# Kernel tuning notes

Hardware: AMD Instinct MI355X
Metric: run time of the kernel (lower is better)

## Reference

```python
import jax, jax.numpy as jnp
import numpy as np

NUM_IMGS = 8192
NUM_CAPS = 8192
R = 7        # views per image
D = 256      # embedding dim


def setup_inputs() -> dict:
    key = jax.random.key(0)
    k1, k2 = jax.random.split(key)
    imgs = jax.random.normal(k1, (NUM_IMGS, R, D), dtype=jnp.float32)
    caps = jax.random.normal(k2, (NUM_CAPS, D), dtype=jnp.float32)
    return {"imgs": imgs, "caps": caps}


def reference(imgs, caps):
    # scores[i, r, c] = <imgs[i, r], caps[c]>  then max over views r
    # matches torch.matmul(imgs, caps.t()).max(1)[0]
    scores = jnp.einsum("ird,cd->irc", imgs, caps)  # [num_imgs, r, num_caps]
    return scores.max(axis=1)                        # [num_imgs, num_caps]
```

## Files before the change

kernel.cpp:

```cpp
#include <hip/hip_runtime.h>
#include <hip/hip_bf16.h>
#include <cstdint>
#include <cstddef>

#define NI 8192
#define NC 8192
#define RV 7
#define DD 256

typedef __bf16 bf16x8 __attribute__((ext_vector_type(8)));
typedef float  f32x4  __attribute__((ext_vector_type(4)));

#define IMGS_WS_BYTES (32u * 56u * 16384u)
#define CAPS_WS_OFF   IMGS_WS_BYTES
#define CAPS_WS_BYTES (64u * 65536u)
#define WS_NEEDED     ((size_t)(IMGS_WS_BYTES + CAPS_WS_BYTES))

static __device__ __forceinline__ unsigned pkbf(float x, float y) {
  unsigned a = __float_as_uint(x) + 0x8000u;
  unsigned b = __float_as_uint(y) + 0x8000u;
  return __builtin_amdgcn_perm(b, a, 0x07060302u);
}

static __device__ __forceinline__ void gload16(const void* g, void* l) {
  __builtin_amdgcn_global_load_lds(
      (const __attribute__((address_space(1))) void*)g,
      (__attribute__((address_space(3))) void*)l, 16, 0, 0);
}

__global__ __launch_bounds__(256)
void conv_imgs(const float* __restrict__ imgs, uint4* __restrict__ ws) {
  unsigned T = blockIdx.x * 256u + threadIdx.x;
  unsigned img = T / 224u;
  unsigned rem = T - img * 224u;
  unsigned r  = rem >> 5;
  unsigned ju = rem & 31u;
  const float* s = imgs + ((size_t)img * RV + r) * DD + ju * 8u;
  float4 a = *(const float4*)s;
  float4 b = *(const float4*)(s + 4);
  uint4 v = { pkbf(a.x, a.y), pkbf(a.z, a.w), pkbf(b.x, b.y), pkbf(b.z, b.w) };
  unsigned ib = img >> 8, lrow = img & 255u;
  unsigned j = ju >> 2, u = ju & 3u;
  unsigned t = r * 8u + j;
  unsigned byteoff = (ib * 56u + t) * 16384u + u * 4096u + lrow * 16u;
  ws[byteoff >> 4] = v;
}

__global__ __launch_bounds__(256)
void conv_caps(const float* __restrict__ caps, uint4* __restrict__ ws) {
  unsigned T = blockIdx.x * 256u + threadIdx.x;
  unsigned gr = T >> 5;
  unsigned ju = T & 31u;
  const float* s = caps + (size_t)gr * DD + ju * 8u;
  float4 a = *(const float4*)s;
  float4 b = *(const float4*)(s + 4);
  uint4 v = { pkbf(a.x, a.y), pkbf(a.z, a.w), pkbf(b.x, b.y), pkbf(b.z, b.w) };
  unsigned cb = gr >> 7, row = gr & 127u;
  unsigned byteoff = cb * 65536u + ju * 2048u + row * 16u;
  ws[byteoff >> 4] = v;
}

__global__ __launch_bounds__(512, 2)
void mvm_mfma(const char* __restrict__ wi, const char* __restrict__ wc,
              float* __restrict__ out)
{
  __shared__ __align__(1024) char lds[65536 + 4 * 16384];
  char* const ldsB = lds;
  char* const ldsA = lds + 65536;

  const int tid  = threadIdx.x;
  const int lane = tid & 63;
  const int wid  = tid >> 6;
  const int wr   = wid >> 1;
  const int wq   = wid & 1;

  const int bid = (int)blockIdx.x;
  const int swz = (bid & 7) * 256 + (bid >> 3);
  const int ib  = swz >> 6;
  const int cb  = swz & 63;

  const char* bsrc  = wc + (size_t)cb * 65536u;
  const char* abase = wi + (size_t)ib * (56u * 16384u);

  #pragma unroll
  for (int l = 0; l < 8; ++l)
    gload16(bsrc + tid * 16 + l * 8192, ldsB + wid * 1024 + l * 8192);
  #pragma unroll
  for (int c = 0; c < 3; ++c) {
    gload16(abase + c * 16384 + tid * 16,        ldsA + c * 16384 + wid * 1024);
    gload16(abase + c * 16384 + tid * 16 + 8192, ldsA + c * 16384 + wid * 1024 + 8192);
  }
  const char* ap = abase + 3 * 16384 + tid * 16;

  asm volatile("s_waitcnt vmcnt(4)" ::: "memory");
  __builtin_amdgcn_s_barrier();
  asm volatile("" ::: "memory");

  const int lrow = lane & 15;
  const int lu   = lane >> 4;
  char* const aB       = ldsA + lu * 4096 + (wr * 64 + lrow) * 16;
  const char* const bB = ldsB + lu * 2048 + (wq * 64 + lrow) * 16;

  f32x4 omax[4][4];
  #pragma unroll
  for (int m = 0; m < 4; ++m)
    #pragma unroll
    for (int n = 0; n < 4; ++n)
      #pragma unroll
      for (int e = 0; e < 4; ++e)
        omax[m][n][e] = -3.4e38f;

  f32x4 acc[4][4];

  for (int i = 0; i < RV; ++i) {
    #pragma unroll
    for (int m = 0; m < 4; ++m)
      #pragma unroll
      for (int n = 0; n < 4; ++n)
        acc[m][n] = (f32x4){0.f, 0.f, 0.f, 0.f};

    #pragma unroll
    for (int j = 0; j < 8; ++j) {
      const int p = j & 3;
      const int q = (j + 3) & 3;

      if (j < 7 || i < 6) {
        gload16(ap,        ldsA + q * 16384 + wid * 1024);
        gload16(ap + 8192, ldsA + q * 16384 + wid * 1024 + 8192);
        ap += 16384;
      }

      bf16x8 a0 = *(const bf16x8*)(aB + p * 16384 + 0 * 256);
      bf16x8 a1 = *(const bf16x8*)(aB + p * 16384 + 1 * 256);
      bf16x8 a2 = *(const bf16x8*)(aB + p * 16384 + 2 * 256);
      bf16x8 a3 = *(const bf16x8*)(aB + p * 16384 + 3 * 256);
      bf16x8 b0 = *(const bf16x8*)(bB + j * 8192 + 0 * 256);
      bf16x8 b1 = *(const bf16x8*)(bB + j * 8192 + 1 * 256);
      bf16x8 b2 = *(const bf16x8*)(bB + j * 8192 + 2 * 256);
      bf16x8 b3 = *(const bf16x8*)(bB + j * 8192 + 3 * 256);

      __builtin_amdgcn_s_barrier();
      asm volatile("" ::: "memory");

      __builtin_amdgcn_s_setprio(1);
      acc[0][0] = __builtin_amdgcn_mfma_f32_16x16x32_bf16(a0, b0, acc[0][0], 0, 0, 0);
      acc[1][0] = __builtin_amdgcn_mfma_f32_16x16x32_bf16(a1, b0, acc[1][0], 0, 0, 0);
      acc[2][0] = __builtin_amdgcn_mfma_f32_16x16x32_bf16(a2, b0, acc[2][0], 0, 0, 0);
      acc[3][0] = __builtin_amdgcn_mfma_f32_16x16x32_bf16(a3, b0, acc[3][0], 0, 0, 0);
      acc[0][1] = __builtin_amdgcn_mfma_f32_16x16x32_bf16(a0, b1, acc[0][1], 0, 0, 0);
      acc[1][1] = __builtin_amdgcn_mfma_f32_16x16x32_bf16(a1, b1, acc[1][1], 0, 0, 0);
      acc[2][1] = __builtin_amdgcn_mfma_f32_16x16x32_bf16(a2, b1, acc[2][1], 0, 0, 0);
      acc[3][1] = __builtin_amdgcn_mfma_f32_16x16x32_bf16(a3, b1, acc[3][1], 0, 0, 0);
      acc[0][2] = __builtin_amdgcn_mfma_f32_16x16x32_bf16(a0, b2, acc[0][2], 0, 0, 0);
      acc[1][2] = __builtin_amdgcn_mfma_f32_16x16x32_bf16(a1, b2, acc[1][2], 0, 0, 0);
      acc[2][2] = __builtin_amdgcn_mfma_f32_16x16x32_bf16(a2, b2, acc[2][2], 0, 0, 0);
      acc[3][2] = __builtin_amdgcn_mfma_f32_16x16x32_bf16(a3, b2, acc[3][2], 0, 0, 0);
      acc[0][3] = __builtin_amdgcn_mfma_f32_16x16x32_bf16(a0, b3, acc[0][3], 0, 0, 0);
      acc[1][3] = __builtin_amdgcn_mfma_f32_16x16x32_bf16(a1, b3, acc[1][3], 0, 0, 0);
      acc[2][3] = __builtin_amdgcn_mfma_f32_16x16x32_bf16(a2, b3, acc[2][3], 0, 0, 0);
      acc[3][3] = __builtin_amdgcn_mfma_f32_16x16x32_bf16(a3, b3, acc[3][3], 0, 0, 0);
      __builtin_amdgcn_s_setprio(0);

      asm volatile("s_waitcnt vmcnt(4)" ::: "memory");
      __builtin_amdgcn_s_barrier();
      asm volatile("" ::: "memory");
    }

    #pragma unroll
    for (int m = 0; m < 4; ++m)
      #pragma unroll
      for (int n = 0; n < 4; ++n)
        #pragma unroll
        for (int e = 0; e < 4; ++e)
          omax[m][n][e] = fmaxf(omax[m][n][e], acc[m][n][e]);
  }

  const int rbase = ib * 256 + wr * 64;
  const int cbase = cb * 128 + wq * 64;
  const int lr4 = (lane >> 4) * 4;
  const int lc  = lane & 15;
  #pragma unroll
  for (int m = 0; m < 4; ++m)
    #pragma unroll
    for (int e = 0; e < 4; ++e) {
      size_t ro = (size_t)(rbase + m * 16 + lr4 + e) * NC;
      #pragma unroll
      for (int n = 0; n < 4; ++n)
        out[ro + cbase + n * 16 + lc] = omax[m][n][e];
    }
}

__global__ __launch_bounds__(512, 1)
void mvm_fallback(const float* __restrict__ imgs, const float* __restrict__ caps,
                  float* __restrict__ out)
{
  __shared__ __align__(16) char ldsB[128 * 512];
  __shared__ __align__(16) char ldsA[2][256 * 128];

  const int tid  = threadIdx.x;
  const int lane = tid & 63;
  const int wid  = tid >> 6;
  const int wr   = wid >> 1;
  const int wc   = wid & 1;
  const int i0   = blockIdx.y * 256;
  const int c0   = blockIdx.x * 128;

  #pragma unroll
  for (int it = 0; it < 8; ++it) {
    int c    = tid + it * 512;
    int row  = c >> 5;
    int colb = (c & 31) * 16;
    const float* p = caps + (size_t)(c0 + row) * DD + (c & 31) * 8;
    float4 a = *(const float4*)p;
    float4 b = *(const float4*)(p + 4);
    uint4 v;
    v.x = pkbf(a.x, a.y); v.y = pkbf(a.z, a.w);
    v.z = pkbf(b.x, b.y); v.w = pkbf(b.z, b.w);
    *(uint4*)(ldsB + row * 512 + (colb ^ ((row & 7) << 4))) = v;
  }
  #pragma unroll
  for (int it = 0; it < 4; ++it) {
    int c    = tid + it * 512;
    int row  = c >> 3;
    int colb = (c & 7) * 16;
    const float* p = imgs + ((size_t)(i0 + row) * RV + 0) * DD + (c & 7) * 8;
    float4 a = *(const float4*)p;
    float4 b = *(const float4*)(p + 4);
    uint4 v;
    v.x = pkbf(a.x, a.y); v.y = pkbf(a.z, a.w);
    v.z = pkbf(b.x, b.y); v.w = pkbf(b.z, b.w);
    *(uint4*)(ldsA[0] + row * 128 + (colb ^ ((row & 7) << 4))) = v;
  }
  __syncthreads();

  f32x4 omax[4][4];
  #pragma unroll
  for (int m = 0; m < 4; ++m)
    #pragma unroll
    for (int n = 0; n < 4; ++n)
      #pragma unroll
      for (int j = 0; j < 4; ++j)
        omax[m][n][j] = -3.4e38f;

  f32x4 acc[4][4];
  int cur = 0;
  const int lrow = lane & 15;
  const int lkb  = (lane >> 4) * 16;

  for (int ch = 0; ch < RV * 4; ++ch) {
    const int kc = ch & 3;
    if (kc == 0) {
      #pragma unroll
      for (int m = 0; m < 4; ++m)
        #pragma unroll
        for (int n = 0; n < 4; ++n)
          acc[m][n] = (f32x4){0.f, 0.f, 0.f, 0.f};
    }
    const int  chn  = ch + 1;
    const bool hasn = (chn < RV * 4);
    float4 pf[8];
    if (hasn) {
      const int rn = chn >> 2;
      const int kn = (chn & 3) * 64;
      #pragma unroll
      for (int it = 0; it < 4; ++it) {
        int c   = tid + it * 512;
        int row = c >> 3;
        const float* p = imgs + ((size_t)(i0 + row) * RV + rn) * DD + kn + (c & 7) * 8;
        pf[2 * it]     = *(const float4*)p;
        pf[2 * it + 1] = *(const float4*)(p + 4);
      }
    }
    #pragma unroll
    for (int ks = 0; ks < 2; ++ks) {
      bf16x8 af[4], bfr[4];
      #pragma unroll
      for (int m = 0; m < 4; ++m) {
        int row = wr * 64 + m * 16 + lrow;
        af[m] = *(const bf16x8*)(ldsA[cur] + row * 128 + ((ks * 64 + lkb) ^ ((row & 7) << 4)));
      }
      #pragma unroll
      for (int n = 0; n < 4; ++n) {
        int row = wc * 64 + n * 16 + lrow;
        bfr[n] = *(const bf16x8*)(ldsB + row * 512 + ((kc * 128 + ks * 64 + lkb) ^ ((row & 7) << 4)));
      }
      #pragma unroll
      for (int m = 0; m < 4; ++m)
        #pragma unroll
        for (int n = 0; n < 4; ++n)
          acc[m][n] = __builtin_amdgcn_mfma_f32_16x16x32_bf16(af[m], bfr[n], acc[m][n], 0, 0, 0);
    }
    if (hasn) {
      #pragma unroll
      for (int it = 0; it < 4; ++it) {
        int c    = tid + it * 512;
        int row  = c >> 3;
        int colb = (c & 7) * 16;
        uint4 v;
        v.x = pkbf(pf[2 * it].x,     pf[2 * it].y);
        v.y = pkbf(pf[2 * it].z,     pf[2 * it].w);
        v.z = pkbf(pf[2 * it + 1].x, pf[2 * it + 1].y);
        v.w = pkbf(pf[2 * it + 1].z, pf[2 * it + 1].w);
        *(uint4*)(ldsA[cur ^ 1] + row * 128 + (colb ^ ((row & 7) << 4))) = v;
      }
    }
    __syncthreads();
    cur ^= 1;
    if (kc == 3) {
      #pragma unroll
      for (int m = 0; m < 4; ++m)
        #pragma unroll
        for (int n = 0; n < 4; ++n)
          #pragma unroll
          for (int j = 0; j < 4; ++j)
            omax[m][n][j] = fmaxf(omax[m][n][j], acc[m][n][j]);
    }
  }

  const int rbase = i0 + wr * 64;
  const int cbase = c0 + wc * 64;
  const int lr4   = (lane >> 4) * 4;
  const int lc    = lane & 15;
  #pragma unroll
  for (int m = 0; m < 4; ++m)
    #pragma unroll
    for (int j = 0; j < 4; ++j) {
      size_t ro = (size_t)(rbase + m * 16 + lr4 + j) * NC;
      #pragma unroll
      for (int n = 0; n < 4; ++n)
        out[ro + cbase + n * 16 + lc] = omax[m][n][j];
    }
}

extern "C" void kernel_launch(void* const* d_in, const int* in_sizes, int n_in,
                              void* d_out, int out_size, void* d_ws, size_t ws_size,
                              hipStream_t stream) {
  const float* imgs = (const float*)d_in[0];
  const float* caps = (const float*)d_in[1];
  float* out = (float*)d_out;

  if (ws_size >= WS_NEEDED) {
    char* ws = (char*)d_ws;
    conv_imgs<<<7168, 256, 0, stream>>>(imgs, (uint4*)ws);
    conv_caps<<<1024, 256, 0, stream>>>(caps, (uint4*)(ws + CAPS_WS_OFF));
    mvm_mfma<<<2048, 512, 0, stream>>>((const char*)ws, (const char*)(ws + CAPS_WS_OFF), out);
  } else {
    dim3 grid(NC / 128, NI / 256);
    mvm_fallback<<<grid, 512, 0, stream>>>(imgs, caps, out);
  }
}
```

Before: 289.3 us.

## Enlarge GEMM tile to 256x256, stream caps via LDS ring, fp16 max accumulators

```diff
diff --git a/kernel.cpp b/kernel.cpp
--- a/kernel.cpp
+++ b/kernel.cpp
@@ -8,12 +8,13 @@
 #define RV 7
 #define DD 256
 
-typedef __bf16 bf16x8 __attribute__((ext_vector_type(8)));
-typedef float  f32x4  __attribute__((ext_vector_type(4)));
+typedef __bf16  bf16x8 __attribute__((ext_vector_type(8)));
+typedef float   f32x4  __attribute__((ext_vector_type(4)));
+typedef __fp16  f16x2  __attribute__((ext_vector_type(2)));
 
 #define IMGS_WS_BYTES (32u * 56u * 16384u)
 #define CAPS_WS_OFF   IMGS_WS_BYTES
-#define CAPS_WS_BYTES (64u * 65536u)
+#define CAPS_WS_BYTES (32u * 8u * 16384u)
 #define WS_NEEDED     ((size_t)(IMGS_WS_BYTES + CAPS_WS_BYTES))
 
 static __device__ __forceinline__ unsigned pkbf(float x, float y) {
@@ -55,66 +56,65 @@
   float4 a = *(const float4*)s;
   float4 b = *(const float4*)(s + 4);
   uint4 v = { pkbf(a.x, a.y), pkbf(a.z, a.w), pkbf(b.x, b.y), pkbf(b.z, b.w) };
-  unsigned cb = gr >> 7, row = gr & 127u;
-  unsigned byteoff = cb * 65536u + ju * 2048u + row * 16u;
+  unsigned cb = gr >> 8, row = gr & 255u;
+  unsigned j = ju >> 2, u = ju & 3u;
+  unsigned byteoff = cb * 131072u + j * 16384u + u * 4096u + row * 16u;
   ws[byteoff >> 4] = v;
 }
 
 __global__ __launch_bounds__(512, 2)
-void mvm_mfma(const char* __restrict__ wi, const char* __restrict__ wc,
+void mvm_mfma(const char* __restrict__ wi, const char* __restrict__ wcap,
               float* __restrict__ out)
 {
-  __shared__ __align__(1024) char lds[65536 + 4 * 16384];
-  char* const ldsB = lds;
-  char* const ldsA = lds + 65536;
+  __shared__ __align__(1024) char lds[131072];
+  char* const ldsA = lds;
+  char* const ldsB = lds + 65536;
 
   const int tid  = threadIdx.x;
   const int lane = tid & 63;
   const int wid  = tid >> 6;
-  const int wr   = wid >> 1;
-  const int wq   = wid & 1;
+  const int wm   = wid >> 2;
+  const int wn   = wid & 3;
 
   const int bid = (int)blockIdx.x;
-  const int swz = (bid & 7) * 256 + (bid >> 3);
-  const int ib  = swz >> 6;
-  const int cb  = swz & 63;
-
-  const char* bsrc  = wc + (size_t)cb * 65536u;
-  const char* abase = wi + (size_t)ib * (56u * 16384u);
-
-  #pragma unroll
-  for (int l = 0; l < 8; ++l)
-    gload16(bsrc + tid * 16 + l * 8192, ldsB + wid * 1024 + l * 8192);
+  const int swz = (bid & 7) * 128 + (bid >> 3);
+  const int ib  = swz >> 5;
+  const int cb  = swz & 31;
+
+  const char* abase = wi   + (size_t)ib * (56u * 16384u);
+  const char* bbase = wcap + (size_t)cb * (8u * 16384u);
+
   #pragma unroll
   for (int c = 0; c < 3; ++c) {
     gload16(abase + c * 16384 + tid * 16,        ldsA + c * 16384 + wid * 1024);
-    gload16(abase + c * 16384 + tid * 16 + 8192, ldsA + c * 16384 + wid * 1024 + 8192);
-  }
-  const char* ap = abase + 3 * 16384 + tid * 16;
-
-  asm volatile("s_waitcnt vmcnt(4)" ::: "memory");
+    gload16(abase + c * 16384 + 8192 + tid * 16, ldsA + c * 16384 + 8192 + wid * 1024);
+    gload16(bbase + c * 16384 + tid * 16,        ldsB + c * 16384 + wid * 1024);
+    gload16(bbase + c * 16384 + 8192 + tid * 16, ldsB + c * 16384 + 8192 + wid * 1024);
+  }
+  asm volatile("s_waitcnt vmcnt(8)" ::: "memory");
   __builtin_amdgcn_s_barrier();
   asm volatile("" ::: "memory");
 
   const int lrow = lane & 15;
   const int lu   = lane >> 4;
-  char* const aB       = ldsA + lu * 4096 + (wr * 64 + lrow) * 16;
-  const char* const bB = ldsB + lu * 2048 + (wq * 64 + lrow) * 16;
-
-  f32x4 omax[4][4];
-  #pragma unroll
-  for (int m = 0; m < 4; ++m)
+  const char* const aB = ldsA + lu * 4096 + (wm * 128 + lrow) * 16;
+  const char* const bB = ldsB + lu * 4096 + (wn * 64  + lrow) * 16;
+  const char* ap = abase + 3 * 16384 + tid * 16;
+
+  f16x2 om[8][4][2];
+  #pragma unroll
+  for (int m = 0; m < 8; ++m)
     #pragma unroll
     for (int n = 0; n < 4; ++n)
       #pragma unroll
-      for (int e = 0; e < 4; ++e)
-        omax[m][n][e] = -3.4e38f;
-
-  f32x4 acc[4][4];
-
-  for (int i = 0; i < RV; ++i) {
-    #pragma unroll
-    for (int m = 0; m < 4; ++m)
+      for (int h = 0; h < 2; ++h)
+        om[m][n][h] = (f16x2){(__fp16)-65504.f, (__fp16)-65504.f};
+
+  f32x4 acc[8][4];
+
+  for (int r = 0; r < RV; ++r) {
+    #pragma unroll
+    for (int m = 0; m < 8; ++m)
       #pragma unroll
       for (int n = 0; n < 4; ++n)
         acc[m][n] = (f32x4){0.f, 0.f, 0.f, 0.f};
@@ -124,23 +124,26 @@
       const int p = j & 3;
       const int q = (j + 3) & 3;
 
-      if (j < 7 || i < 6) {
-        gload16(ap,        ldsA + q * 16384 + wid * 1024);
-        gload16(ap + 8192, ldsA + q * 16384 + wid * 1024 + 8192);
-        ap += 16384;
-      }
-
+      gload16(ap,        ldsA + q * 16384 + wid * 1024);
+      gload16(ap + 8192, ldsA + q * 16384 + 8192 + wid * 1024);
+      gload16(bbase + ((j + 3) & 7) * 16384 + tid * 16,
+              ldsB + q * 16384 + wid * 1024);
+      gload16(bbase + ((j + 3) & 7) * 16384 + 8192 + tid * 16,
+              ldsB + q * 16384 + 8192 + wid * 1024);
+      ap += 16384;
+
+      bf16x8 b0 = *(const bf16x8*)(bB + p * 16384 + 0 * 256);
+      bf16x8 b1 = *(const bf16x8*)(bB + p * 16384 + 1 * 256);
+      bf16x8 b2 = *(const bf16x8*)(bB + p * 16384 + 2 * 256);
+      bf16x8 b3 = *(const bf16x8*)(bB + p * 16384 + 3 * 256);
       bf16x8 a0 = *(const bf16x8*)(aB + p * 16384 + 0 * 256);
       bf16x8 a1 = *(const bf16x8*)(aB + p * 16384 + 1 * 256);
       bf16x8 a2 = *(const bf16x8*)(aB + p * 16384 + 2 * 256);
       bf16x8 a3 = *(const bf16x8*)(aB + p * 16384 + 3 * 256);
-      bf16x8 b0 = *(const bf16x8*)(bB + j * 8192 + 0 * 256);
-      bf16x8 b1 = *(const bf16x8*)(bB + j * 8192 + 1 * 256);
-      bf16x8 b2 = *(const bf16x8*)(bB + j * 8192 + 2 * 256);
-      bf16x8 b3 = *(const bf16x8*)(bB + j * 8192 + 3 * 256);
-
-      __builtin_amdgcn_s_barrier();
-      asm volatile("" ::: "memory");
+      bf16x8 a4 = *(const bf16x8*)(aB + p * 16384 + 4 * 256);
+      bf16x8 a5 = *(const bf16x8*)(aB + p * 16384 + 5 * 256);
+      bf16x8 a6 = *(const bf16x8*)(aB + p * 16384 + 6 * 256);
+      bf16x8 a7 = *(const bf16x8*)(aB + p * 16384 + 7 * 256);
 
       __builtin_amdgcn_s_setprio(1);
       acc[0][0] = __builtin_amdgcn_mfma_f32_16x16x32_bf16(a0, b0, acc[0][0], 0, 0, 0);
@@ -161,33 +164,54 @@
       acc[3][3] = __builtin_amdgcn_mfma_f32_16x16x32_bf16(a3, b3, acc[3][3], 0, 0, 0);
       __builtin_amdgcn_s_setprio(0);
 
-      asm volatile("s_waitcnt vmcnt(4)" ::: "memory");
+      __builtin_amdgcn_s_setprio(1);
+      acc[4][0] = __builtin_amdgcn_mfma_f32_16x16x32_bf16(a4, b0, acc[4][0], 0, 0, 0);
+      acc[5][0] = __builtin_amdgcn_mfma_f32_16x16x32_bf16(a5, b0, acc[5][0], 0, 0, 0);
+      acc[6][0] = __builtin_amdgcn_mfma_f32_16x16x32_bf16(a6, b0, acc[6][0], 0, 0, 0);
+      acc[7][0] = __builtin_amdgcn_mfma_f32_16x16x32_bf16(a7, b0, acc[7][0], 0, 0, 0);
+      acc[4][1] = __builtin_amdgcn_mfma_f32_16x16x32_bf16(a4, b1, acc[4][1], 0, 0, 0);
+      acc[5][1] = __builtin_amdgcn_mfma_f32_16x16x32_bf16(a5, b1, acc[5][1], 0, 0, 0);
+      acc[6][1] = __builtin_amdgcn_mfma_f32_16x16x32_bf16(a6, b1, acc[6][1], 0, 0, 0);
+      acc[7][1] = __builtin_amdgcn_mfma_f32_16x16x32_bf16(a7, b1, acc[7][1], 0, 0, 0);
+      acc[4][2] = __builtin_amdgcn_mfma_f32_16x16x32_bf16(a4, b2, acc[4][2], 0, 0, 0);
+      acc[5][2] = __builtin_amdgcn_mfma_f32_16x16x32_bf16(a5, b2, acc[5][2], 0, 0, 0);
+      acc[6][2] = __builtin_amdgcn_mfma_f32_16x16x32_bf16(a6, b2, acc[6][2], 0, 0, 0);
+      acc[7][2] = __builtin_amdgcn_mfma_f32_16x16x32_bf16(a7, b2, acc[7][2], 0, 0, 0);
+      acc[4][3] = __builtin_amdgcn_mfma_f32_16x16x32_bf16(a4, b3, acc[4][3], 0, 0, 0);
+      acc[5][3] = __builtin_amdgcn_mfma_f32_16x16x32_bf16(a5, b3, acc[5][3], 0, 0, 0);
+      acc[6][3] = __builtin_amdgcn_mfma_f32_16x16x32_bf16(a6, b3, acc[6][3], 0, 0, 0);
+      acc[7][3] = __builtin_amdgcn_mfma_f32_16x16x32_bf16(a7, b3, acc[7][3], 0, 0, 0);
+      __builtin_amdgcn_s_setprio(0);
+
+      asm volatile("s_waitcnt vmcnt(8)" ::: "memory");
       __builtin_amdgcn_s_barrier();
       asm volatile("" ::: "memory");
     }
 
     #pragma unroll
-    for (int m = 0; m < 4; ++m)
-      #pragma unroll
-      for (int n = 0; n < 4; ++n)
+    for (int m = 0; m < 8; ++m)
+      #pragma unroll
+      for (int n = 0; n < 4; ++n) {
+        f16x2 lo = __builtin_amdgcn_cvt_pkrtz(acc[m][n][0], acc[m][n][1]);
+        f16x2 hi = __builtin_amdgcn_cvt_pkrtz(acc[m][n][2], acc[m][n][3]);
+        om[m][n][0] = __builtin_elementwise_max(om[m][n][0], lo);
+        om[m][n][1] = __builtin_elementwise_max(om[m][n][1], hi);
+      }
+  }
+
+  const int rbase = ib * 256 + wm * 128;
+  const int cbase = cb * 256 + wn * 64;
+  #pragma unroll
+  for (int m = 0; m < 8; ++m)
+    #pragma unroll
+    for (int h = 0; h < 2; ++h)
+      #pragma unroll
+      for (int e = 0; e < 2; ++e) {
+        size_t ro = (size_t)(rbase + m * 16 + lu * 4 + h * 2 + e) * NC + cbase + lrow;
         #pragma unroll
-        for (int e = 0; e < 4; ++e)
-          omax[m][n][e] = fmaxf(omax[m][n][e], acc[m][n][e]);
-  }
-
-  const int rbase = ib * 256 + wr * 64;
-  const int cbase = cb * 128 + wq * 64;
-  const int lr4 = (lane >> 4) * 4;
-  const int lc  = lane & 15;
-  #pragma unroll
-  for (int m = 0; m < 4; ++m)
-    #pragma unroll
-    for (int e = 0; e < 4; ++e) {
-      size_t ro = (size_t)(rbase + m * 16 + lr4 + e) * NC;
-      #pragma unroll
-      for (int n = 0; n < 4; ++n)
-        out[ro + cbase + n * 16 + lc] = omax[m][n][e];
-    }
+        for (int n = 0; n < 4; ++n)
+          out[ro + n * 16] = (float)om[m][n][h][e];
+      }
 }
 
 __global__ __launch_bounds__(512, 1)
@@ -282,7 +306,7 @@
       #pragma unroll
       for (int n = 0; n < 4; ++n) {
         int row = wc * 64 + n * 16 + lrow;
-        bfr[n] = *(const bf16x8*)(ldsB + row * 512 + ((kc * 128 + ks * 64 + lkb) ^ ((row & 7) << 4)));
+        bfr[n] = *(const bf16x8*)(ldsB + row * 512 + (((ch & 3) * 128 + ks * 64 + lkb) ^ ((row & 7) << 4)));
       }
       #pragma unroll
       for (int m = 0; m < 4; ++m)
@@ -343,7 +367,7 @@
     char* ws = (char*)d_ws;
     conv_imgs<<<7168, 256, 0, stream>>>(imgs, (uint4*)ws);
     conv_caps<<<1024, 256, 0, stream>>>(caps, (uint4*)(ws + CAPS_WS_OFF));
-    mvm_mfma<<<2048, 512, 0, stream>>>((const char*)ws, (const char*)(ws + CAPS_WS_OFF), out);
+    mvm_mfma<<<1024, 512, 0, stream>>>((const char*)ws, (const char*)(ws + CAPS_WS_OFF), out);
   } else {
     dim3 grid(NC / 128, NI / 256);
     mvm_fallback<<<grid, 512, 0, stream>>>(imgs, caps, out);
```

Measured after the change: 375.8 us. 1.3x slower.
